# Kernel tuning notes

Hardware: AMD Instinct MI355X
Metric: run time of the kernel (lower is better)

The kernel has to match this reference:

```python
import jax, jax.numpy as jnp
import numpy as np

N_NODES = 50000
N_EDGES = 800000
IN_CH = 128
HIDDEN = 64
OUT_CH = 32
N_REL = 8
N_GRAPHS = 64
NEG_SLOPE = 0.2  # RGATConv default leaky_relu slope


def setup_inputs() -> dict:
    key = jax.random.key(0)
    ks = jax.random.split(key, 20)
    s = 0.05
    inp = {
        "x": jax.random.normal(ks[0], (N_NODES, IN_CH), dtype=jnp.float32),
        "edge_index": jax.random.randint(ks[1], (2, N_EDGES), 0, N_NODES, dtype=jnp.int64),
        "edge_type": jax.random.randint(ks[2], (N_EDGES,), 0, N_REL, dtype=jnp.int64),
        "batch": jnp.sort(jax.random.randint(ks[3], (N_NODES,), 0, N_GRAPHS, dtype=jnp.int64)),
        # encoder Linear(in, hidden)
        "enc_W": jax.random.normal(ks[4], (IN_CH, HIDDEN), dtype=jnp.float32) * s,
        "enc_b": jnp.zeros((HIDDEN,), dtype=jnp.float32),
        # RGAT layer 0 (hidden -> hidden), heads=1, dim=1
        "w0": jax.random.normal(ks[5], (N_REL, HIDDEN, HIDDEN), dtype=jnp.float32) * s,
        "q0": jax.random.normal(ks[6], (HIDDEN, 1), dtype=jnp.float32) * s,
        "k0": jax.random.normal(ks[7], (HIDDEN, 1), dtype=jnp.float32) * s,
        "b0": jnp.zeros((HIDDEN,), dtype=jnp.float32),
        # RGAT layer 1 (hidden -> hidden)
        "w1": jax.random.normal(ks[8], (N_REL, HIDDEN, HIDDEN), dtype=jnp.float32) * s,
        "q1": jax.random.normal(ks[9], (HIDDEN, 1), dtype=jnp.float32) * s,
        "k1": jax.random.normal(ks[10], (HIDDEN, 1), dtype=jnp.float32) * s,
        "b1": jnp.zeros((HIDDEN,), dtype=jnp.float32),
        # head: Linear(hidden, hidden) + ReLU, then clf Linear(hidden, out)
        "lin_W": jax.random.normal(ks[11], (HIDDEN, HIDDEN), dtype=jnp.float32) * s,
        "lin_b": jnp.zeros((HIDDEN,), dtype=jnp.float32),
        "clf_W": jax.random.normal(ks[12], (HIDDEN, OUT_CH), dtype=jnp.float32) * s,
        "clf_b": jnp.zeros((OUT_CH,), dtype=jnp.float32),
    }
    return inp


def rgat_layer(h, src, dst, etype, w, q, k, b):
    # per-relation transform of all nodes: [R, N, out]
    h_all = jnp.einsum('ni,rio->rno', h, w)
    hi = h_all[etype, dst]          # [E, out] transformed target feats
    hj = h_all[etype, src]          # [E, out] transformed source feats
    # additive self-attention (heads=1, dim=1), across-relation softmax
    alpha = jax.nn.leaky_relu((hi @ q + hj @ k)[:, 0], NEG_SLOPE)  # [E]
    m = jax.ops.segment_max(alpha, dst, num_segments=N_NODES)
    e = jnp.exp(alpha - m[dst])
    ssum = jax.ops.segment_sum(e, dst, num_segments=N_NODES)
    a = e / jnp.maximum(ssum[dst], 1e-16)
    out = jax.ops.segment_sum(a[:, None] * hj, dst, num_segments=N_NODES)
    return out + b


def reference(x, edge_index, edge_type, batch,
              enc_W, enc_b, w0, q0, k0, b0, w1, q1, k1, b1,
              lin_W, lin_b, clf_W, clf_b):
    src, dst = edge_index[0], edge_index[1]
    h = x @ enc_W + enc_b                      # encoder
    h = rgat_layer(h, src, dst, edge_type, w0, q0, k0, b0)
    h = jax.nn.relu(h)                         # inter-layer relu (dropout=0)
    h = rgat_layer(h, src, dst, edge_type, w1, q1, k1, b1)
    pooled = jax.ops.segment_sum(h, batch, num_segments=N_GRAPHS)  # global_add_pool
    z = jax.nn.relu(pooled @ lin_W + lin_b)
    return z @ clf_W + clf_b                   # [N_GRAPHS, OUT_CH]
```

## Files before the change

### kernel.cpp

```cpp
#include <hip/hip_runtime.h>
#include <hip/hip_bf16.h>

#define NN 50000
#define NE 800000
#define INC 128
#define HID 64
#define OUTC 32
#define NREL 8
#define NG 64
#define SLOPE 0.2f
#define NB2 196
#define SCAP 6144

typedef unsigned int uint32;
typedef unsigned short ushort16;
typedef __attribute__((ext_vector_type(8))) short short8;
typedef __attribute__((ext_vector_type(4))) short short4v;
typedef __attribute__((ext_vector_type(4))) float float4v;
typedef __attribute__((ext_vector_type(4))) int int4v;

__device__ __forceinline__ float bf2f(ushort16 u) {
    union { uint32 i; float f; } v; v.i = ((uint32)u) << 16; return v.f;
}
__device__ __forceinline__ ushort16 f2bf(float f) {
    union { float f; uint32 i; } v; v.f = f;
    uint32 i = v.i;
    return (ushort16)((i + 0x7FFFu + ((i >> 16) & 1u)) >> 16);
}

__global__ __launch_bounds__(256) void enc_mfma(const float* __restrict__ x,
    const float* __restrict__ W, const float* __restrict__ bias,
    ushort16* __restrict__ hb)
{
    int tid = threadIdx.x, wv = tid >> 6, lane = tid & 63;
    int g = lane >> 4, lr = lane & 15;

    short8 bf[4][4];
    for (int t = 0; t < 4; ++t)
        for (int kc = 0; kc < 4; ++kc) {
            short8 v;
            #pragma unroll
            for (int j = 0; j < 8; ++j) {
                int k = kc * 32 + g * 8 + j;
                v[j] = (short)f2bf(W[k * HID + t * 16 + lr]);
            }
            bf[t][kc] = v;
        }

    __shared__ float lds[4][16 * 65];
    float* myl = lds[wv];

    for (int tile = blockIdx.x * 4 + wv; tile < NN / 16; tile += gridDim.x * 4) {
        int row0 = tile * 16;
        const float4v* xp = (const float4v*)(x + (size_t)(row0 + lr) * INC);
        short8 af[4];
        #pragma unroll
        for (int kc = 0; kc < 4; ++kc) {
            float4v u0 = xp[kc * 8 + g * 2];
            float4v u1 = xp[kc * 8 + g * 2 + 1];
            short8 v;
            v[0] = (short)f2bf(u0[0]); v[1] = (short)f2bf(u0[1]);
            v[2] = (short)f2bf(u0[2]); v[3] = (short)f2bf(u0[3]);
            v[4] = (short)f2bf(u1[0]); v[5] = (short)f2bf(u1[1]);
            v[6] = (short)f2bf(u1[2]); v[7] = (short)f2bf(u1[3]);
            af[kc] = v;
        }
        float4v acc[4];
        #pragma unroll
        for (int t = 0; t < 4; ++t) { float4v z = {0.f,0.f,0.f,0.f}; acc[t] = z; }
        #pragma unroll
        for (int t = 0; t < 4; ++t)
            #pragma unroll
            for (int kc = 0; kc < 4; ++kc)
                acc[t] = __builtin_amdgcn_mfma_f32_16x16x32_bf16(af[kc], bf[t][kc], acc[t], 0, 0, 0);

        #pragma unroll
        for (int t = 0; t < 4; ++t)
            #pragma unroll
            for (int i = 0; i < 4; ++i)
                myl[(4 * g + i) * 65 + t * 16 + lr] = acc[t][i];
        __asm volatile("s_waitcnt lgkmcnt(0)" ::: "memory");

        int row = lane >> 2, cg = lane & 3;
        const float* srcp = myl + row * 65 + cg * 16;
        uint32 p[8];
        #pragma unroll
        for (int j = 0; j < 8; ++j) {
            float v0 = srcp[2 * j]     + bias[cg * 16 + 2 * j];
            float v1 = srcp[2 * j + 1] + bias[cg * 16 + 2 * j + 1];
            p[j] = (uint32)f2bf(v0) | ((uint32)f2bf(v1) << 16);
        }
        int4v s0 = {(int)p[0], (int)p[1], (int)p[2], (int)p[3]};
        int4v s1 = {(int)p[4], (int)p[5], (int)p[6], (int)p[7]};
        int4v* op = (int4v*)(hb + (size_t)(row0 + row) * HID + cg * 16);
        op[0] = s0; op[1] = s1;
        __asm volatile("s_waitcnt lgkmcnt(0)" ::: "memory");
    }
}

__global__ __launch_bounds__(256) void hall_mfma(const ushort16* __restrict__ hb,
    const float* __restrict__ w, ushort16* __restrict__ hall)
{
    int r = blockIdx.y;
    int tid = threadIdx.x, wv = tid >> 6, lane = tid & 63;
    int g = lane >> 4, lr = lane & 15;
    const float* wr = w + (size_t)r * HID * HID;

    short8 bf[4][2];
    for (int t = 0; t < 4; ++t)
        for (int kc = 0; kc < 2; ++kc) {
            short8 v;
            #pragma unroll
            for (int j = 0; j < 8; ++j) {
                int k = kc * 32 + g * 8 + j;
                v[j] = (short)f2bf(wr[k * HID + t * 16 + lr]);
            }
            bf[t][kc] = v;
        }

    __shared__ float lds[4][16 * 65];
    float* myl = lds[wv];
    ushort16* outr = hall + (size_t)r * NN * HID;

    for (int tile = blockIdx.x * 4 + wv; tile < NN / 16; tile += gridDim.x * 4) {
        int row0 = tile * 16;
        const short8* ap = (const short8*)(hb + (size_t)(row0 + lr) * HID);
        short8 a0 = ap[g];
        short8 a1 = ap[4 + g];
        float4v acc[4];
        #pragma unroll
        for (int t = 0; t < 4; ++t) { float4v z = {0.f,0.f,0.f,0.f}; acc[t] = z; }
        #pragma unroll
        for (int t = 0; t < 4; ++t) {
            acc[t] = __builtin_amdgcn_mfma_f32_16x16x32_bf16(a0, bf[t][0], acc[t], 0, 0, 0);
            acc[t] = __builtin_amdgcn_mfma_f32_16x16x32_bf16(a1, bf[t][1], acc[t], 0, 0, 0);
        }
        #pragma unroll
        for (int t = 0; t < 4; ++t)
            #pragma unroll
            for (int i = 0; i < 4; ++i)
                myl[(4 * g + i) * 65 + t * 16 + lr] = acc[t][i];
        __asm volatile("s_waitcnt lgkmcnt(0)" ::: "memory");

        int row = lane >> 2, cg = lane & 3;
        const float* srcp = myl + row * 65 + cg * 16;
        uint32 p[8];
        #pragma unroll
        for (int j = 0; j < 8; ++j)
            p[j] = (uint32)f2bf(srcp[2 * j]) | ((uint32)f2bf(srcp[2 * j + 1]) << 16);
        int4v s0 = {(int)p[0], (int)p[1], (int)p[2], (int)p[3]};
        int4v s1 = {(int)p[4], (int)p[5], (int)p[6], (int)p[7]};
        int4v* op = (int4v*)(outr + (size_t)(row0 + row) * HID + cg * 16);
        __builtin_nontemporal_store(s0, op);
        __builtin_nontemporal_store(s1, op + 1);
        __asm volatile("s_waitcnt lgkmcnt(0)" ::: "memory");
    }
}

__global__ __launch_bounds__(256) void prep_kernel(
    const float* __restrict__ w0, const float* __restrict__ q0, const float* __restrict__ k0,
    const float* __restrict__ w1, const float* __restrict__ q1, const float* __restrict__ k1,
    float* __restrict__ wqk0, float* __restrict__ wqk1,
    int* __restrict__ bucketHist)
{
    int b = blockIdx.x, t = threadIdx.x;
    if (b < 32) {
        const float* w  = (b < 16) ? w0 : w1;
        const float* qv = (b < 16) ? q0 : q1;
        const float* kv = (b < 16) ? k0 : k1;
        float* out = (b < 16) ? wqk0 : wqk1;
        int j = b & 15;
        int r = j & 7;
        const float* vv = (j < 8) ? qv : kv;
        if (t < 64) {
            const float* wr = w + ((size_t)r * HID + t) * HID;
            float acc = 0.f;
            for (int o = 0; o < HID; ++o) acc += wr[o] * vv[o];
            out[j * HID + t] = acc;
        }
    } else {
        if (t < NB2) bucketHist[t] = 0;
    }
}

__global__ __launch_bounds__(256) void s_kernel(const ushort16* __restrict__ hb,
    const float* __restrict__ wqk, float* __restrict__ sbuf)
{
    __shared__ float Ws[16 * 65];
    __shared__ short4v Hs[16][17];
    int tid = threadIdx.x;
    for (int i = tid; i < 16 * HID; i += 256) Ws[(i >> 6) * 65 + (i & 63)] = wqk[i];
    int n0 = blockIdx.x * 16;
    {
        int row = tid >> 4, ch = tid & 15;
        Hs[row][ch] = *(const short4v*)(hb + (size_t)(n0 + row) * HID + ch * 4);
    }
    __syncthreads();
    int j = tid & 15, nl = tid >> 4;
    short4v hreg[16];
    #pragma unroll
    for (int c = 0; c < 16; ++c) hreg[c] = Hs[nl][c];
    float acc = 0.f;
    #pragma unroll
    for (int c = 0; c < 16; ++c)
        #pragma unroll
        for (int u = 0; u < 4; ++u)
            acc += bf2f((ushort16)hreg[c][u]) * Ws[j * 65 + c * 4 + u];
    sbuf[(size_t)j * NN + n0 + nl] = acc;
}

__global__ __launch_bounds__(256) void histo196(const int* __restrict__ dst,
                                                int* __restrict__ bucketHist)
{
    __shared__ int lh[NB2];
    int t = threadIdx.x;
    for (int i = t; i < NB2; i += 256) lh[i] = 0;
    __syncthreads();
    int base = blockIdx.x * 2048;
    for (int i = t; i < 2048; i += 256) {
        int idx = base + i;
        if (idx < NE) atomicAdd(&lh[dst[idx] >> 8], 1);
    }
    __syncthreads();
    for (int i = t; i < NB2; i += 256) if (lh[i]) atomicAdd(&bucketHist[i], lh[i]);
}

__global__ __launch_bounds__(256) void scan196(const int* __restrict__ bucketHist,
    int* __restrict__ bucketBase, int* __restrict__ bucket_cur,
    float* __restrict__ pooled)
{
    __shared__ int ps[256];
    int t = threadIdx.x;
    int v = (t < NB2) ? bucketHist[t] : 0;
    ps[t] = v;
    __syncthreads();
    for (int off = 1; off < 256; off <<= 1) {
        int tv = (t >= off) ? ps[t - off] : 0;
        __syncthreads();
        ps[t] += tv;
        __syncthreads();
    }
    int excl = ps[t] - v;
    if (t < NB2) { bucketBase[t] = excl; bucket_cur[t] = excl; }
    if (t == 0) bucketBase[NB2] = NE;
    #pragma unroll
    for (int i = 0; i < (NG * HID) / 256; ++i) pooled[i * 256 + t] = 0.f;
}

__global__ __launch_bounds__(256) void binpass(const int* __restrict__ src,
    const int* __restrict__ dst, const int* __restrict__ et,
    int* __restrict__ bucket_cur, uint32* __restrict__ ebin)
{
    __shared__ int lh[NB2], lbase[NB2], lcur[NB2];
    int t = threadIdx.x;
    for (int i = t; i < NB2; i += 256) { lh[i] = 0; lcur[i] = 0; }
    __syncthreads();
    int base = blockIdx.x * 4096;
    uint32 rec[16]; int bkt[16];
    #pragma unroll
    for (int i = 0; i < 16; ++i) {
        int idx = base + i * 256 + t;
        bkt[i] = -1;
        if (idx < NE) {
            int s = src[idx], d = dst[idx], r = et[idx];
            rec[i] = (uint32)s | ((uint32)r << 16) | ((uint32)(d & 255) << 19);
            bkt[i] = d >> 8;
            atomicAdd(&lh[bkt[i]], 1);
        }
    }
    __syncthreads();
    for (int i = t; i < NB2; i += 256) if (lh[i]) lbase[i] = atomicAdd(&bucket_cur[i], lh[i]);
    __syncthreads();
    #pragma unroll
    for (int i = 0; i < 16; ++i) {
        if (bkt[i] >= 0) {
            int lpos = atomicAdd(&lcur[bkt[i]], 1);
            ebin[lbase[bkt[i]] + lpos] = rec[i];
        }
    }
}

__global__ __launch_bounds__(256) void sortpass(const uint32* __restrict__ ebin,
    const int* __restrict__ bucketBase, int* __restrict__ rowptr,
    uint32* __restrict__ edges_s)
{
    __shared__ uint32 stage[SCAP];
    __shared__ int cnt256[256], ps[256], cur[256];
    int b = blockIdx.x, t = threadIdx.x;
    int seg0 = bucketBase[b], seg1 = bucketBase[b + 1];
    int cnt = seg1 - seg0;
    cnt256[t] = 0;
    __syncthreads();
    for (int i = t; i < cnt; i += 256) {
        uint32 rec = ebin[seg0 + i];
        atomicAdd(&cnt256[(rec >> 19) & 255], 1);
    }
    __syncthreads();
    int v = cnt256[t];
    ps[t] = v;
    __syncthreads();
    for (int off = 1; off < 256; off <<= 1) {
        int tv = (t >= off) ? ps[t - off] : 0;
        __syncthreads();
        ps[t] += tv;
        __syncthreads();
    }
    int excl = ps[t] - v;
    int node = (b << 8) + t;
    if (node < NN) rowptr[node] = seg0 + excl;
    if (b == NB2 - 1 && t == 0) rowptr[NN] = NE;
    cur[t] = excl;
    __syncthreads();
    for (int i = t; i < cnt; i += 256) {
        uint32 rec = ebin[seg0 + i];
        int lpos = atomicAdd(&cur[(rec >> 19) & 255], 1);
        if (lpos < SCAP) stage[lpos] = rec;
        else edges_s[seg0 + lpos] = rec;
    }
    __syncthreads();
    int lim = cnt < SCAP ? cnt : SCAP;
    for (int i = t; i < lim; i += 256) edges_s[seg0 + i] = stage[i];
}

__global__ __launch_bounds__(256) void agg_kernel(const int* __restrict__ rowptr,
    const uint32* __restrict__ edges, const float* __restrict__ sbuf,
    const ushort16* __restrict__ hall, const float* __restrict__ bias,
    ushort16* __restrict__ out_bf, float* __restrict__ out_f32, int do_relu)
{
    int wv = threadIdx.x >> 6, lane = threadIdx.x & 63;
    int d = blockIdx.x * 4 + wv;
    if (d >= NN) return;
    int row0 = rowptr[d];
    int deg = rowptr[d + 1] - row0;
    int g = lane >> 3, cl = lane & 7;

    float myq = (lane < 8) ? sbuf[lane * NN + d] : 0.f;

    float acc[8];
    #pragma unroll
    for (int u = 0; u < 8; ++u) acc[u] = 0.f;
    float ssum = 0.f;

    for (int base = 0; base < deg; base += 32) {
        int j0 = base + g;
        bool v0 = j0      < deg, v1 = j0 + 8  < deg;
        bool v2 = j0 + 16 < deg, v3 = j0 + 24 < deg;
        uint32 pk0 = v0 ? edges[row0 + j0]      : 0u;
        uint32 pk1 = v1 ? edges[row0 + j0 + 8]  : 0u;
        uint32 pk2 = v2 ? edges[row0 + j0 + 16] : 0u;
        uint32 pk3 = v3 ? edges[row0 + j0 + 24] : 0u;
        int s0 = (int)(pk0 & 0xFFFFu), r0 = (int)((pk0 >> 16) & 7u);
        int s1 = (int)(pk1 & 0xFFFFu), r1 = (int)((pk1 >> 16) & 7u);
        int s2 = (int)(pk2 & 0xFFFFu), r2 = (int)((pk2 >> 16) & 7u);
        int s3 = (int)(pk3 & 0xFFFFu), r3 = (int)((pk3 >> 16) & 7u);
        float sc0 = sbuf[(8 + r0) * NN + s0];
        float sc1 = sbuf[(8 + r1) * NN + s1];
        float sc2 = sbuf[(8 + r2) * NN + s2];
        float sc3 = sbuf[(8 + r3) * NN + s3];
        short8 hv0 = *(const short8*)(hall + ((size_t)r0 * NN + s0) * HID + cl * 8);
        short8 hv1 = *(const short8*)(hall + ((size_t)r1 * NN + s1) * HID + cl * 8);
        short8 hv2 = *(const short8*)(hall + ((size_t)r2 * NN + s2) * HID + cl * 8);
        short8 hv3 = *(const short8*)(hall + ((size_t)r3 * NN + s3) * HID + cl * 8);
        float a0 = __shfl(myq, r0) + sc0; a0 = (a0 > 0.f) ? a0 : SLOPE * a0;
        float a1 = __shfl(myq, r1) + sc1; a1 = (a1 > 0.f) ? a1 : SLOPE * a1;
        float a2 = __shfl(myq, r2) + sc2; a2 = (a2 > 0.f) ? a2 : SLOPE * a2;
        float a3 = __shfl(myq, r3) + sc3; a3 = (a3 > 0.f) ? a3 : SLOPE * a3;
        float ex0 = v0 ? __expf(a0) : 0.f;
        float ex1 = v1 ? __expf(a1) : 0.f;
        float ex2 = v2 ? __expf(a2) : 0.f;
        float ex3 = v3 ? __expf(a3) : 0.f;
        ssum += (ex0 + ex1) + (ex2 + ex3);
        #pragma unroll
        for (int u = 0; u < 8; ++u)
            acc[u] += (ex0 * bf2f((ushort16)hv0[u]) + ex1 * bf2f((ushort16)hv1[u]))
                    + (ex2 * bf2f((ushort16)hv2[u]) + ex3 * bf2f((ushort16)hv3[u]));
    }

    #pragma unroll
    for (int o = 8; o < 64; o <<= 1) {
        ssum += __shfl_xor(ssum, o);
        #pragma unroll
        for (int u = 0; u < 8; ++u) acc[u] += __shfl_xor(acc[u], o);
    }

    if (lane < 8) {
        float inv = 1.f / fmaxf(ssum, 1e-16f);
        float o_[8];
        #pragma unroll
        for (int u = 0; u < 8; ++u) o_[u] = acc[u] * inv + bias[lane * 8 + u];
        if (do_relu) {
            uint32 p[4];
            #pragma unroll
            for (int u = 0; u < 4; ++u) {
                float v0 = fmaxf(o_[2 * u], 0.f);
                float v1 = fmaxf(o_[2 * u + 1], 0.f);
                p[u] = (uint32)f2bf(v0) | ((uint32)f2bf(v1) << 16);
            }
            int4v pk4 = {(int)p[0], (int)p[1], (int)p[2], (int)p[3]};
            *(int4v*)(out_bf + (size_t)d * HID + lane * 8) = pk4;
        } else {
            float4v v0 = {o_[0], o_[1], o_[2], o_[3]};
            float4v v1 = {o_[4], o_[5], o_[6], o_[7]};
            float4v* op = (float4v*)(out_f32 + (size_t)d * HID + lane * 8);
            op[0] = v0; op[1] = v1;
        }
    }
}

__global__ void pool_kernel(const float* __restrict__ h, const int* __restrict__ batch,
                            float* __restrict__ pooled)
{
    int t = blockIdx.x * 256 + threadIdx.x;
    int c = t & 63;
    int chunk = t >> 6;
    if (chunk >= NN / 16) return;
    int n0 = chunk * 16;
    float acc = 0.f;
    int cur = batch[n0];
    for (int n = n0; n < n0 + 16; ++n) {
        int b = batch[n];
        if (b != cur) { atomicAdd(&pooled[cur * HID + c], acc); acc = 0.f; cur = b; }
        acc += h[(size_t)n * HID + c];
    }
    atomicAdd(&pooled[cur * HID + c], acc);
}

__global__ __launch_bounds__(256) void head_kernel(const float* __restrict__ pooled,
    const float* __restrict__ linW, const float* __restrict__ linb,
    const float* __restrict__ clfW, const float* __restrict__ clfb,
    float* __restrict__ out)
{
    __shared__ float z[NG * HID];
    __shared__ float p[NG * HID];
    int tid = threadIdx.x;
    for (int i = tid; i < NG * HID; i += 256) p[i] = pooled[i];
    __syncthreads();
    for (int idx = tid; idx < NG * HID; idx += 256) {
        int g = idx >> 6, c = idx & 63;
        float acc = linb[c];
        for (int k = 0; k < HID; ++k) acc += p[g * HID + k] * linW[k * HID + c];
        z[idx] = fmaxf(acc, 0.f);
    }
    __syncthreads();
    for (int idx = tid; idx < NG * OUTC; idx += 256) {
        int g = idx >> 5, c = idx & 31;
        float acc = clfb[c];
        for (int k = 0; k < HID; ++k) acc += z[g * HID + k] * clfW[k * OUTC + c];
        out[idx] = acc;
    }
}

extern "C" void kernel_launch(void* const* d_in, const int* in_sizes, int n_in,
                              void* d_out, int out_size, void* d_ws, size_t ws_size,
                              hipStream_t stream)
{
    const float* x      = (const float*)d_in[0];
    const int*   eidx   = (const int*)d_in[1];
    const int*   etype  = (const int*)d_in[2];
    const int*   batch  = (const int*)d_in[3];
    const float* enc_W  = (const float*)d_in[4];
    const float* enc_b  = (const float*)d_in[5];
    const float* w0     = (const float*)d_in[6];
    const float* q0     = (const float*)d_in[7];
    const float* k0     = (const float*)d_in[8];
    const float* b0     = (const float*)d_in[9];
    const float* w1     = (const float*)d_in[10];
    const float* q1     = (const float*)d_in[11];
    const float* k1     = (const float*)d_in[12];
    const float* b1     = (const float*)d_in[13];
    const float* lin_W  = (const float*)d_in[14];
    const float* lin_b  = (const float*)d_in[15];
    const float* clf_W  = (const float*)d_in[16];
    const float* clf_b  = (const float*)d_in[17];

    const int* srcp = eidx;
    const int* dstp = eidx + NE;

    char* wsb = (char*)d_ws;
    ushort16* h_bf    = (ushort16*)wsb;                 wsb += (size_t)NN * HID * 2;
    ushort16* hall_bf = (ushort16*)wsb;                 wsb += (size_t)NREL * NN * HID * 2;
    float*    h_f     = (float*)wsb;                    wsb += (size_t)NN * HID * 4;
    float*    sbuf    = (float*)wsb;                    wsb += (size_t)16 * NN * 4;
    float*    wqk0    = (float*)wsb;                    wsb += 16 * HID * 4;
    float*    wqk1    = (float*)wsb;                    wsb += 16 * HID * 4;
    float*    pooled  = (float*)wsb;                    wsb += NG * HID * 4;
    int*      rowptr  = (int*)wsb;                      wsb += (size_t)(NN + 64) * 4;
    int*      bucketHist = (int*)wsb;                   wsb += 256 * 4;
    int*      bucketBase = (int*)wsb;                   wsb += 256 * 4;
    int*      bucket_cur = (int*)wsb;                   wsb += 256 * 4;
    uint32*   ebin    = (uint32*)wsb;                   wsb += (size_t)NE * 4;
    uint32*   edges_s = (uint32*)wsb;                   wsb += (size_t)(NE + 64) * 4;

    prep_kernel<<<33, 256, 0, stream>>>(w0, q0, k0, w1, q1, k1, wqk0, wqk1, bucketHist);

    histo196<<<(NE + 2047) / 2048, 256, 0, stream>>>(dstp, bucketHist);
    scan196<<<1, 256, 0, stream>>>(bucketHist, bucketBase, bucket_cur, pooled);
    binpass<<<(NE + 4095) / 4096, 256, 0, stream>>>(srcp, dstp, etype, bucket_cur, ebin);
    sortpass<<<NB2, 256, 0, stream>>>(ebin, bucketBase, rowptr, edges_s);

    enc_mfma<<<512, 256, 0, stream>>>(x, enc_W, enc_b, h_bf);

    s_kernel<<<NN / 16, 256, 0, stream>>>(h_bf, wqk0, sbuf);
    hall_mfma<<<dim3(512, NREL), 256, 0, stream>>>(h_bf, w0, hall_bf);
    agg_kernel<<<(NN + 3) / 4, 256, 0, stream>>>(rowptr, edges_s, sbuf, hall_bf, b0,
                                                 h_bf, (float*)nullptr, 1);

    s_kernel<<<NN / 16, 256, 0, stream>>>(h_bf, wqk1, sbuf);
    hall_mfma<<<dim3(512, NREL), 256, 0, stream>>>(h_bf, w1, hall_bf);
    agg_kernel<<<(NN + 3) / 4, 256, 0, stream>>>(rowptr, edges_s, sbuf, hall_bf, b1,
                                                 (ushort16*)nullptr, h_f, 0);

    pool_kernel<<<(NN / 16 * HID + 255) / 256, 256, 0, stream>>>(h_f, batch, pooled);
    head_kernel<<<1, 256, 0, stream>>>(pooled, lin_W, lin_b, clf_W, clf_b, (float*)d_out);
}
```

Before: 195.6 us.

## Merge score and relation-transform kernels; shrink aggregation unroll; drop nontemporal stores

```diff
diff --git a/kernel.cpp b/kernel.cpp
--- a/kernel.cpp
+++ b/kernel.cpp
@@ -11,6 +11,7 @@
 #define SLOPE 0.2f
 #define NB2 196
 #define SCAP 6144
+#define S_BLOCKS (NN / 16)
 
 typedef unsigned int uint32;
 typedef unsigned short ushort16;
@@ -98,15 +99,44 @@
     }
 }
 
-__global__ __launch_bounds__(256) void hall_mfma(const ushort16* __restrict__ hb,
-    const float* __restrict__ w, ushort16* __restrict__ hall)
-{
-    int r = blockIdx.y;
-    int tid = threadIdx.x, wv = tid >> 6, lane = tid & 63;
+__global__ __launch_bounds__(256) void sh_kernel(const ushort16* __restrict__ hb,
+    const float* __restrict__ wqk, const float* __restrict__ w,
+    float* __restrict__ sbuf, ushort16* __restrict__ hall)
+{
+    __shared__ float lds4[4][16 * 65];
+    __shared__ float Ws[16 * 65];
+    __shared__ short4v Hs[16][17];
+    int tid = threadIdx.x;
+
+    if (blockIdx.x < S_BLOCKS) {
+        for (int i = tid; i < 16 * HID; i += 256) Ws[(i >> 6) * 65 + (i & 63)] = wqk[i];
+        int n0 = blockIdx.x * 16;
+        {
+            int row = tid >> 4, ch = tid & 15;
+            Hs[row][ch] = *(const short4v*)(hb + (size_t)(n0 + row) * HID + ch * 4);
+        }
+        __syncthreads();
+        int j = tid & 15, nl = tid >> 4;
+        short4v hreg[16];
+        #pragma unroll
+        for (int c = 0; c < 16; ++c) hreg[c] = Hs[nl][c];
+        float acc = 0.f;
+        #pragma unroll
+        for (int c = 0; c < 16; ++c)
+            #pragma unroll
+            for (int u = 0; u < 4; ++u)
+                acc += bf2f((ushort16)hreg[c][u]) * Ws[j * 65 + c * 4 + u];
+        sbuf[(size_t)j * NN + n0 + nl] = acc;
+        return;
+    }
+
+    int b = blockIdx.x - S_BLOCKS;
+    int r = b >> 9, xb = b & 511;
+    int wv = tid >> 6, lane = tid & 63;
     int g = lane >> 4, lr = lane & 15;
     const float* wr = w + (size_t)r * HID * HID;
 
-    short8 bf[4][2];
+    short8 bfr[4][2];
     for (int t = 0; t < 4; ++t)
         for (int kc = 0; kc < 2; ++kc) {
             short8 v;
@@ -115,14 +145,13 @@
                 int k = kc * 32 + g * 8 + j;
                 v[j] = (short)f2bf(wr[k * HID + t * 16 + lr]);
             }
-            bf[t][kc] = v;
-        }
-
-    __shared__ float lds[4][16 * 65];
-    float* myl = lds[wv];
+            bfr[t][kc] = v;
+        }
+
+    float* myl = lds4[wv];
     ushort16* outr = hall + (size_t)r * NN * HID;
 
-    for (int tile = blockIdx.x * 4 + wv; tile < NN / 16; tile += gridDim.x * 4) {
+    for (int tile = xb * 4 + wv; tile < NN / 16; tile += 512 * 4) {
         int row0 = tile * 16;
         const short8* ap = (const short8*)(hb + (size_t)(row0 + lr) * HID);
         short8 a0 = ap[g];
@@ -132,8 +161,8 @@
         for (int t = 0; t < 4; ++t) { float4v z = {0.f,0.f,0.f,0.f}; acc[t] = z; }
         #pragma unroll
         for (int t = 0; t < 4; ++t) {
-            acc[t] = __builtin_amdgcn_mfma_f32_16x16x32_bf16(a0, bf[t][0], acc[t], 0, 0, 0);
-            acc[t] = __builtin_amdgcn_mfma_f32_16x16x32_bf16(a1, bf[t][1], acc[t], 0, 0, 0);
+            acc[t] = __builtin_amdgcn_mfma_f32_16x16x32_bf16(a0, bfr[t][0], acc[t], 0, 0, 0);
+            acc[t] = __builtin_amdgcn_mfma_f32_16x16x32_bf16(a1, bfr[t][1], acc[t], 0, 0, 0);
         }
         #pragma unroll
         for (int t = 0; t < 4; ++t)
@@ -151,8 +180,7 @@
         int4v s0 = {(int)p[0], (int)p[1], (int)p[2], (int)p[3]};
         int4v s1 = {(int)p[4], (int)p[5], (int)p[6], (int)p[7]};
         int4v* op = (int4v*)(outr + (size_t)(row0 + row) * HID + cg * 16);
-        __builtin_nontemporal_store(s0, op);
-        __builtin_nontemporal_store(s1, op + 1);
+        op[0] = s0; op[1] = s1;
         __asm volatile("s_waitcnt lgkmcnt(0)" ::: "memory");
     }
 }
@@ -183,32 +211,6 @@
     }
 }
 
-__global__ __launch_bounds__(256) void s_kernel(const ushort16* __restrict__ hb,
-    const float* __restrict__ wqk, float* __restrict__ sbuf)
-{
-    __shared__ float Ws[16 * 65];
-    __shared__ short4v Hs[16][17];
-    int tid = threadIdx.x;
-    for (int i = tid; i < 16 * HID; i += 256) Ws[(i >> 6) * 65 + (i & 63)] = wqk[i];
-    int n0 = blockIdx.x * 16;
-    {
-        int row = tid >> 4, ch = tid & 15;
-        Hs[row][ch] = *(const short4v*)(hb + (size_t)(n0 + row) * HID + ch * 4);
-    }
-    __syncthreads();
-    int j = tid & 15, nl = tid >> 4;
-    short4v hreg[16];
-    #pragma unroll
-    for (int c = 0; c < 16; ++c) hreg[c] = Hs[nl][c];
-    float acc = 0.f;
-    #pragma unroll
-    for (int c = 0; c < 16; ++c)
-        #pragma unroll
-        for (int u = 0; u < 4; ++u)
-            acc += bf2f((ushort16)hreg[c][u]) * Ws[j * 65 + c * 4 + u];
-    sbuf[(size_t)j * NN + n0 + nl] = acc;
-}
-
 __global__ __launch_bounds__(256) void histo196(const int* __restrict__ dst,
                                                 int* __restrict__ bucketHist)
 {
@@ -341,39 +343,25 @@
     for (int u = 0; u < 8; ++u) acc[u] = 0.f;
     float ssum = 0.f;
 
-    for (int base = 0; base < deg; base += 32) {
-        int j0 = base + g;
-        bool v0 = j0      < deg, v1 = j0 + 8  < deg;
-        bool v2 = j0 + 16 < deg, v3 = j0 + 24 < deg;
-        uint32 pk0 = v0 ? edges[row0 + j0]      : 0u;
-        uint32 pk1 = v1 ? edges[row0 + j0 + 8]  : 0u;
-        uint32 pk2 = v2 ? edges[row0 + j0 + 16] : 0u;
-        uint32 pk3 = v3 ? edges[row0 + j0 + 24] : 0u;
+    for (int base = 0; base < deg; base += 16) {
+        int j0 = base + g, j1 = j0 + 8;
+        bool v0 = j0 < deg, v1 = j1 < deg;
+        uint32 pk0 = v0 ? edges[row0 + j0] : 0u;
+        uint32 pk1 = v1 ? edges[row0 + j1] : 0u;
         int s0 = (int)(pk0 & 0xFFFFu), r0 = (int)((pk0 >> 16) & 7u);
         int s1 = (int)(pk1 & 0xFFFFu), r1 = (int)((pk1 >> 16) & 7u);
-        int s2 = (int)(pk2 & 0xFFFFu), r2 = (int)((pk2 >> 16) & 7u);
-        int s3 = (int)(pk3 & 0xFFFFu), r3 = (int)((pk3 >> 16) & 7u);
         float sc0 = sbuf[(8 + r0) * NN + s0];
         float sc1 = sbuf[(8 + r1) * NN + s1];
-        float sc2 = sbuf[(8 + r2) * NN + s2];
-        float sc3 = sbuf[(8 + r3) * NN + s3];
         short8 hv0 = *(const short8*)(hall + ((size_t)r0 * NN + s0) * HID + cl * 8);
         short8 hv1 = *(const short8*)(hall + ((size_t)r1 * NN + s1) * HID + cl * 8);
-        short8 hv2 = *(const short8*)(hall + ((size_t)r2 * NN + s2) * HID + cl * 8);
-        short8 hv3 = *(const short8*)(hall + ((size_t)r3 * NN + s3) * HID + cl * 8);
         float a0 = __shfl(myq, r0) + sc0; a0 = (a0 > 0.f) ? a0 : SLOPE * a0;
         float a1 = __shfl(myq, r1) + sc1; a1 = (a1 > 0.f) ? a1 : SLOPE * a1;
-        float a2 = __shfl(myq, r2) + sc2; a2 = (a2 > 0.f) ? a2 : SLOPE * a2;
-        float a3 = __shfl(myq, r3) + sc3; a3 = (a3 > 0.f) ? a3 : SLOPE * a3;
         float ex0 = v0 ? __expf(a0) : 0.f;
         float ex1 = v1 ? __expf(a1) : 0.f;
-        float ex2 = v2 ? __expf(a2) : 0.f;
-        float ex3 = v3 ? __expf(a3) : 0.f;
-        ssum += (ex0 + ex1) + (ex2 + ex3);
+        ssum += ex0 + ex1;
         #pragma unroll
         for (int u = 0; u < 8; ++u)
-            acc[u] += (ex0 * bf2f((ushort16)hv0[u]) + ex1 * bf2f((ushort16)hv1[u]))
-                    + (ex2 * bf2f((ushort16)hv2[u]) + ex3 * bf2f((ushort16)hv3[u]));
+            acc[u] += ex0 * bf2f((ushort16)hv0[u]) + ex1 * bf2f((ushort16)hv1[u]);
     }
 
     #pragma unroll
@@ -500,13 +488,13 @@
 
     enc_mfma<<<512, 256, 0, stream>>>(x, enc_W, enc_b, h_bf);
 
-    s_kernel<<<NN / 16, 256, 0, stream>>>(h_bf, wqk0, sbuf);
-    hall_mfma<<<dim3(512, NREL), 256, 0, stream>>>(h_bf, w0, hall_bf);
+    const int SH_GRID = S_BLOCKS + 512 * NREL;
+
+    sh_kernel<<<SH_GRID, 256, 0, stream>>>(h_bf, wqk0, w0, sbuf, hall_bf);
     agg_kernel<<<(NN + 3) / 4, 256, 0, stream>>>(rowptr, edges_s, sbuf, hall_bf, b0,
                                                  h_bf, (float*)nullptr, 1);
 
-    s_kernel<<<NN / 16, 256, 0, stream>>>(h_bf, wqk1, sbuf);
-    hall_mfma<<<dim3(512, NREL), 256, 0, stream>>>(h_bf, w1, hall_bf);
+    sh_kernel<<<SH_GRID, 256, 0, stream>>>(h_bf, wqk1, w1, sbuf, hall_bf);
     agg_kernel<<<(NN + 3) / 4, 256, 0, stream>>>(rowptr, edges_s, sbuf, hall_bf, b1,
                                                  (ushort16*)nullptr, h_f, 0);
 
```

New measurement: 183.6 us. -6.1%, faster.
